# Kernel tuning notes

Hardware: AMD Instinct MI355X
Metric: run time of the kernel (lower is better)

The kernel has to match this reference:

```python
import jax, jax.numpy as jnp
import numpy as np
import math

B, S, E, H = 2, 2048, 1024, 16
D = E // H
EPS = 1e-5


def setup_inputs() -> dict:
    key = jax.random.key(0)
    ks = jax.random.split(key, 6)
    s = 1.0 / math.sqrt(E)
    return {
        "query": jax.random.normal(ks[0], (B, S, E), jnp.float32),
        "Wq": jax.random.normal(ks[1], (E, E), jnp.float32) * s,
        "bq": jnp.zeros((E,), jnp.float32),
        "Wk": jax.random.normal(ks[2], (E, E), jnp.float32) * s,
        "bk": jnp.zeros((E,), jnp.float32),
        "Wv": jax.random.normal(ks[3], (E, E), jnp.float32) * s,
        "bv": jnp.zeros((E,), jnp.float32),
        "Wo": jax.random.normal(ks[4], (E, E), jnp.float32) * s,
        "bo": jnp.zeros((E,), jnp.float32),
        "alpha": jnp.ones((1,), jnp.float32),
    }


def reference(query, Wq, bq, Wk, bk, Wv, bv, Wo, bo, alpha):
    # Q/K/V projections (nn.Linear: x @ W.T + b)
    q = (query @ Wq.T + bq).reshape(B, S, H, D)
    k = (query @ Wk.T + bk).reshape(B, S, H, D)
    v = (query @ Wv.T + bv).reshape(B, S, H, D)

    # YAT scores: (q.k)^2 / (||q-k||^2 + eps)
    qk = jnp.einsum('bqhd,bkhd->bhqk', q, k)          # [B,H,S,S]
    sq = jnp.einsum('bqhd,bqhd->bhq', q, q)           # ||q||^2
    sk = jnp.einsum('bkhd,bkhd->bhk', k, k)           # ||k||^2
    dist_sq = sq[..., :, None] + sk[..., None, :] - 2.0 * qk
    scores = (qk * qk) / (dist_sq + EPS)

    # learnable alpha scaling: scores * (sqrt(d)/log(1+d))^alpha
    scale = (jnp.sqrt(jnp.float32(D)) / jnp.log1p(jnp.float32(D))) ** alpha[0]
    scores = scores * scale

    attn = jax.nn.softmax(scores, axis=-1)
    out = jnp.einsum('bhqk,bkhd->bqhd', attn, v).reshape(B, S, E)
    return out @ Wo.T + bo
```

## Files before the change

kernel.cpp:

```cpp
#include <hip/hip_runtime.h>
#include <hip/hip_fp16.h>
#include <math.h>

#define BB 2
#define SS 2048
#define EE 1024
#define HH 16
#define DD 64
#define YAT_EPS 1e-5f
#define RR (BB * HH * SS)

typedef __attribute__((ext_vector_type(8))) short bf16x8;
typedef __attribute__((ext_vector_type(4))) short short4v;
typedef __attribute__((ext_vector_type(4))) float f32x4;
#define MFMA16(a, b, c) __builtin_amdgcn_mfma_f32_16x16x32_bf16((a), (b), (c), 0, 0, 0)

#if __has_builtin(__builtin_amdgcn_exp2f)
#define EXP2(x) __builtin_amdgcn_exp2f(x)
#else
#define EXP2(x) exp2f(x)
#endif
#if __has_builtin(__builtin_amdgcn_rcpf)
#define RCPF(x) __builtin_amdgcn_rcpf(x)
#else
#define RCPF(x) (1.0f / (x))
#endif

__device__ __forceinline__ unsigned short f2bf(float x) {
    unsigned int u = __float_as_uint(x);
    u += 0x7FFFu + ((u >> 16) & 1u);
    return (unsigned short)(u >> 16);
}
__device__ __forceinline__ float bf2f(unsigned short h) {
    return __uint_as_float(((unsigned int)h) << 16);
}
__device__ __forceinline__ short f2bf_t(float x) {
    return (short)(__float_as_uint(x) >> 16);
}

__device__ __forceinline__ void async_ld16(void* lds, const void* g) {
    __builtin_amdgcn_global_load_lds(
        (const __attribute__((address_space(1))) unsigned int*)g,
        (__attribute__((address_space(3))) unsigned int*)lds, 16, 0, 0);
}

__global__ __launch_bounds__(256) void split_f32(const float* __restrict__ in,
                                                 unsigned short* __restrict__ hi,
                                                 unsigned short* __restrict__ lo,
                                                 int n4) {
    int i = blockIdx.x * 256 + threadIdx.x;
    if (i >= n4) return;
    float4 v = ((const float4*)in)[i];
    ushort4 h, l;
    h.x = f2bf(v.x); l.x = f2bf(v.x - bf2f(h.x));
    h.y = f2bf(v.y); l.y = f2bf(v.y - bf2f(h.y));
    h.z = f2bf(v.z); l.z = f2bf(v.z - bf2f(h.z));
    h.w = f2bf(v.w); l.w = f2bf(v.w - bf2f(h.w));
    ((ushort4*)hi)[i] = h;
    ((ushort4*)lo)[i] = l;
}

__global__ __launch_bounds__(256) void split_w4(
        const float* __restrict__ Wq, const float* __restrict__ Wk,
        const float* __restrict__ Wv, const float* __restrict__ Wo,
        unsigned short* __restrict__ Whi, unsigned short* __restrict__ Wlo,
        unsigned short* __restrict__ Wohi) {
    int i = blockIdx.x * 256 + threadIdx.x;
    int y = blockIdx.y;
    const float* src = y == 0 ? Wq : y == 1 ? Wk : y == 2 ? Wv : Wo;
    unsigned short* hi = y < 3 ? Whi + (size_t)y * EE * EE : Wohi;
    float4 v = ((const float4*)src)[i];
    ushort4 h;
    h.x = f2bf(v.x); h.y = f2bf(v.y); h.z = f2bf(v.z); h.w = f2bf(v.w);
    ((ushort4*)hi)[i] = h;
    if (y < 2) {
        unsigned short* lo = Wlo + (size_t)y * EE * EE;
        ushort4 l;
        l.x = f2bf(v.x - bf2f(h.x));
        l.y = f2bf(v.y - bf2f(h.y));
        l.z = f2bf(v.z - bf2f(h.z));
        l.w = f2bf(v.w - bf2f(h.w));
        ((ushort4*)lo)[i] = l;
    }
}

__global__ __launch_bounds__(256, 2) void proj_qkv(
        const unsigned short* __restrict__ Ahi, const unsigned short* __restrict__ Alo,
        const unsigned short* __restrict__ Whi, const unsigned short* __restrict__ Wlo,
        const float* __restrict__ bq, const float* __restrict__ bk,
        const float* __restrict__ bv,
        unsigned short* __restrict__ qhi, unsigned short* __restrict__ qlo,
        unsigned short* __restrict__ khi, unsigned short* __restrict__ vt,
        float* __restrict__ sqn, float* __restrict__ skn) {
    __shared__ __align__(16) unsigned short SH[128 * 136];
    unsigned short* LA_hi = SH;
    unsigned short* LA_lo = SH + 4096;
    unsigned short* LB_hi = SH + 8192;
    unsigned short* LB_lo = SH + 12288;

    const int K = EE;
    const int t = threadIdx.x;
    const int w = t >> 6, lane = t & 63;
    const int quad = lane >> 4, lr = lane & 15;
    const int wy = w & 1, wx = w >> 1;
    const bool p3 = blockIdx.x < 16;
    const int m0 = blockIdx.y * 128;
    const int n0 = p3 ? blockIdx.x * 128 : 0;
    const int c0 = p3 ? 0 : (blockIdx.x - 16) * 128;

    const unsigned short* gsrc = nullptr;
    unsigned short* ldst = nullptr;
    if (w == 0)      { gsrc = Ahi + (size_t)m0 * K; ldst = LA_hi; }
    else if (w == 2) {
        gsrc = p3 ? Whi + (size_t)n0 * K
                  : Whi + (size_t)(2 * EE + c0) * K;
        ldst = LB_hi;
    } else if (p3 && w == 1) { gsrc = Alo + (size_t)m0 * K; ldst = LA_lo; }
    else if (p3 && w == 3)   { gsrc = Wlo + (size_t)n0 * K; ldst = LB_lo; }
    const unsigned short* gl = gsrc ? gsrc + (size_t)(lane >> 2) * K + (lane & 3) * 8
                                    : nullptr;

    f32x4 acc[4][4];
    #pragma unroll
    for (int i = 0; i < 4; ++i)
        #pragma unroll
        for (int j = 0; j < 4; ++j)
            acc[i][j] = (f32x4){0.f, 0.f, 0.f, 0.f};

    for (int k0 = 0; k0 < K; k0 += 32) {
        __syncthreads();
        if (gl) {
            #pragma unroll
            for (int i = 0; i < 8; ++i)
                async_ld16(ldst + i * 512, gl + (size_t)i * 16 * K + k0);
        }
        __syncthreads();
        bf16x8 ah[4], al[4], bh_[4], bl_[4];
        #pragma unroll
        for (int i = 0; i < 4; ++i) {
            ah[i]  = *(const bf16x8*)&LA_hi[(wy * 64 + i * 16 + lr) * 32 + quad * 8];
            bh_[i] = *(const bf16x8*)&LB_hi[(wx * 64 + i * 16 + lr) * 32 + quad * 8];
            if (p3) {
                al[i]  = *(const bf16x8*)&LA_lo[(wy * 64 + i * 16 + lr) * 32 + quad * 8];
                bl_[i] = *(const bf16x8*)&LB_lo[(wx * 64 + i * 16 + lr) * 32 + quad * 8];
            }
        }
        #pragma unroll
        for (int mg = 0; mg < 4; ++mg)
            #pragma unroll
            for (int ns = 0; ns < 4; ++ns) {
                f32x4 a = acc[mg][ns];
                a = MFMA16(ah[mg], bh_[ns], a);
                if (p3) {
                    a = MFMA16(ah[mg], bl_[ns], a);
                    a = MFMA16(al[mg], bh_[ns], a);
                }
                acc[mg][ns] = a;
            }
    }

    if (p3) {
        const int ng = n0 + wx * 64;
        const int path = ng >> 10;
        const int c = ng & 1023;
        const int h = c >> 6;
        const float* bias = path == 0 ? bq : bk;
        unsigned short* hi_p = path == 0 ? qhi : khi;
        float* nrm = path == 0 ? sqn : skn;
        float bias_v[4];
        #pragma unroll
        for (int ns = 0; ns < 4; ++ns) bias_v[ns] = bias[c + ns * 16 + lr];
        #pragma unroll
        for (int mg = 0; mg < 4; ++mg)
            #pragma unroll
            for (int r = 0; r < 4; ++r) {
                int m = m0 + wy * 64 + mg * 16 + quad * 4 + r;
                int b = m >> 11, s = m & (SS - 1);
                size_t base = ((size_t)(b * HH + h) * SS + s) * DD;
                float v4[4];
                #pragma unroll
                for (int ns = 0; ns < 4; ++ns) v4[ns] = acc[mg][ns][r] + bias_v[ns];
                float pn = v4[0] * v4[0] + v4[1] * v4[1] + v4[2] * v4[2] + v4[3] * v4[3];
                #pragma unroll
                for (int off = 1; off < 16; off <<= 1) pn += __shfl_xor(pn, off);
                if (lr == 0) nrm[(size_t)(b * HH + h) * SS + s] = pn;
                #pragma unroll
                for (int ns = 0; ns < 4; ++ns) {
                    unsigned short hv = f2bf(v4[ns]);
                    hi_p[base + ns * 16 + lr] = hv;
                    if (path == 0)
                        qlo[base + ns * 16 + lr] = f2bf(v4[ns] - bf2f(hv));
                }
            }
    } else {
        __syncthreads();
        float bias_v[4];
        #pragma unroll
        for (int ns = 0; ns < 4; ++ns) bias_v[ns] = bv[c0 + wx * 64 + ns * 16 + lr];
        #pragma unroll
        for (int mg = 0; mg < 4; ++mg)
            #pragma unroll
            for (int r = 0; r < 4; ++r) {
                int mloc = wy * 64 + mg * 16 + quad * 4 + r;
                #pragma unroll
                for (int ns = 0; ns < 4; ++ns) {
                    int cloc = wx * 64 + ns * 16 + lr;
                    SH[cloc * 136 + mloc] = f2bf(acc[mg][ns][r] + bias_v[ns]);
                }
            }
        __syncthreads();
        const int b = m0 >> 11, s0 = m0 & (SS - 1);
        #pragma unroll
        for (int jc = 0; jc < 8; ++jc) {
            int cl = (t >> 4) + jc * 16;
            int sl = (t & 15) * 8;
            bf16x8 vv = *(const bf16x8*)&SH[cl * 136 + sl];
            int c = c0 + cl, h = c >> 6, d = c & 63;
            *(bf16x8*)&vt[((size_t)(b * HH + h) * DD + d) * SS + s0 + sl] = vv;
        }
    }
}

template <int MODE, int PASSES>
__global__ __launch_bounds__(256, 2) void gemm3p(
        const unsigned short* __restrict__ Ahi, const unsigned short* __restrict__ Alo,
        const unsigned short* __restrict__ Bhi, const unsigned short* __restrict__ Blo,
        const float* __restrict__ bq,
        float* __restrict__ Cf,
        int M, int N, int K) {
    __shared__ __align__(16) unsigned short LA_hi[128 * 32];
    __shared__ __align__(16) unsigned short LB_hi[128 * 32];

    const int t = threadIdx.x;
    const int w = t >> 6, lane = t & 63;
    const int quad = lane >> 4, lr = lane & 15;
    const int wy = w & 1, wx = w >> 1;
    const int m0 = blockIdx.y * 128, n0 = blockIdx.x * 128;

    const unsigned short* gsrc = nullptr;
    unsigned short* ldst = nullptr;
    if (w == 0)      { gsrc = Ahi + (size_t)m0 * K; ldst = LA_hi; }
    else if (w == 2) { gsrc = Bhi + (size_t)n0 * K; ldst = LB_hi; }
    const unsigned short* gl = gsrc ? gsrc + (size_t)(lane >> 2) * K + (lane & 3) * 8
                                    : nullptr;

    f32x4 acc[4][4];
    #pragma unroll
    for (int i = 0; i < 4; ++i)
        #pragma unroll
        for (int j = 0; j < 4; ++j)
            acc[i][j] = (f32x4){0.f, 0.f, 0.f, 0.f};

    for (int k0 = 0; k0 < K; k0 += 32) {
        __syncthreads();
        if (gl) {
            #pragma unroll
            for (int i = 0; i < 8; ++i)
                async_ld16(ldst + i * 512, gl + (size_t)i * 16 * K + k0);
        }
        __syncthreads();
        bf16x8 ah[4], bh_[4];
        #pragma unroll
        for (int i = 0; i < 4; ++i) {
            ah[i]  = *(const bf16x8*)&LA_hi[(wy * 64 + i * 16 + lr) * 32 + quad * 8];
            bh_[i] = *(const bf16x8*)&LB_hi[(wx * 64 + i * 16 + lr) * 32 + quad * 8];
        }
        #pragma unroll
        for (int mg = 0; mg < 4; ++mg)
            #pragma unroll
            for (int ns = 0; ns < 4; ++ns)
                acc[mg][ns] = MFMA16(ah[mg], bh_[ns], acc[mg][ns]);
    }

    const int ng = n0 + wx * 64;
    float bias_v[4];
    #pragma unroll
    for (int ns = 0; ns < 4; ++ns) bias_v[ns] = bq[ng + ns * 16 + lr];
    #pragma unroll
    for (int mg = 0; mg < 4; ++mg)
        #pragma unroll
        for (int r = 0; r < 4; ++r) {
            int m = m0 + wy * 64 + mg * 16 + quad * 4 + r;
            #pragma unroll
            for (int ns = 0; ns < 4; ++ns)
                Cf[(size_t)m * N + ng + ns * 16 + lr] = acc[mg][ns][r] + bias_v[ns];
        }
}

__global__ __launch_bounds__(256, 4) void yat_attn_mfma(
        const unsigned short* __restrict__ qhi, const unsigned short* __restrict__ qlo,
        const unsigned short* __restrict__ khi,
        const unsigned short* __restrict__ vt,
        const float* __restrict__ sqn, const float* __restrict__ skn,
        const float* __restrict__ alphap,
        __half* __restrict__ Opart, float2* __restrict__ mlpart) {
    __shared__ __align__(16) unsigned short Ks[2][4096];
    __shared__ __align__(16) unsigned short Ps[4][16 * 68];

    const int t = threadIdx.x;
    const int w = t >> 6, lane = t & 63;
    const int quad = lane >> 4, lr = lane & 15;
    const int qt = blockIdx.x, bh = blockIdx.y, z = blockIdx.z;
    const int row0 = qt * 64 + w * 16;
    const float cscale = powf(sqrtf((float)DD) / log1pf((float)DD), alphap[0])
                         * 1.4426950408889634f;

    bf16x8 qh[2], ql[2];
    #pragma unroll
    for (int kd = 0; kd < 2; ++kd) {
        size_t o = ((size_t)bh * SS + row0 + lr) * DD + kd * 32 + quad * 8;
        qh[kd] = *(const bf16x8*)&qhi[o];
        ql[kd] = *(const bf16x8*)&qlo[o];
    }
    const float sqe = sqn[(size_t)bh * SS + row0 + lr] + YAT_EPS;

    const int lrow = lane >> 3;
    const int lofs = lrow * 64 + (((lane & 7) ^ (lrow & 7)) << 3);
    const int sw = lr & 7;

    float m_r = -INFINITY, l_r = 0.f;
    f32x4 O[4];
    #pragma unroll
    for (int nd = 0; nd < 4; ++nd) O[nd] = (f32x4){0.f, 0.f, 0.f, 0.f};

    const int t0 = z * 16;
    const size_t khi_base = (size_t)bh * SS * 64 + (size_t)w * 16 * 64 + lofs;
    const size_t skn_base = (size_t)bh * SS + quad * 4;
    unsigned short* myP = Ps[w];

    #pragma unroll
    for (int i2 = 0; i2 < 2; ++i2)
        async_ld16(&Ks[0][w * 1024 + i2 * 512],
                   khi + khi_base + (size_t)t0 * 4096 + i2 * 512);

    for (int it = 0; it < 16; ++it) {
        const int p = it & 1;
        __syncthreads();
        if (it + 1 < 16) {
            #pragma unroll
            for (int i2 = 0; i2 < 2; ++i2)
                async_ld16(&Ks[p ^ 1][w * 1024 + i2 * 512],
                           khi + khi_base + (size_t)(t0 + it + 1) * 4096 + i2 * 512);
        }
        const int kbase = (t0 + it) * 64;
        const unsigned short* kb = Ks[p];
        f32x4 acc[4];
        f32x4 sk4[4];
        #pragma unroll
        for (int st = 0; st < 4; ++st) {
            const int rbase = (st * 16 + lr) * 64;
            bf16x8 kh0 = *(const bf16x8*)&kb[rbase + ((quad    ) ^ sw) * 8];
            bf16x8 kh1 = *(const bf16x8*)&kb[rbase + ((quad + 4) ^ sw) * 8];
            sk4[st] = *(const f32x4*)&skn[skn_base + kbase + st * 16];
            f32x4 a = (f32x4){0.f, 0.f, 0.f, 0.f};
            a = MFMA16(kh0, qh[0], a);
            a = MFMA16(kh1, qh[1], a);
            a = MFMA16(kh0, ql[0], a);
            a = MFMA16(kh1, ql[1], a);
            acc[st] = a;
        }
        bf16x8 vf[4][2];
        #pragma unroll
        for (int nd = 0; nd < 4; ++nd)
            #pragma unroll
            for (int kk = 0; kk < 2; ++kk)
                vf[nd][kk] = *(const bf16x8*)&vt[((size_t)bh * DD + nd * 16 + lr) * SS
                                                 + kbase + kk * 32 + quad * 8];
        float mx = -INFINITY;
        #pragma unroll
        for (int st = 0; st < 4; ++st)
            #pragma unroll
            for (int r = 0; r < 4; ++r) {
                float qk = acc[st][r];
                float d = sqe + sk4[st][r] - 2.f * qk;
                float u = qk * qk * RCPF(d);
                acc[st][r] = u;
                mx = fmaxf(mx, u);
            }
        mx = fmaxf(mx, __shfl_xor(mx, 16));
        mx = fmaxf(mx, __shfl_xor(mx, 32));
        float mnew = fmaxf(m_r, mx);
        bool resc = !__all(cscale * (mnew - m_r) <= 8.f);
        float aa = 1.f;
        if (resc) {
            aa = EXP2(__builtin_fmaf(cscale, m_r, -cscale * mnew));
            m_r = mnew;
        }
        const float cm = cscale * m_r;
        float rs = 0.f;
        #pragma unroll
        for (int st = 0; st < 4; ++st) {
            float e0 = EXP2(__builtin_fmaf(cscale, acc[st][0], -cm));
            float e1 = EXP2(__builtin_fmaf(cscale, acc[st][1], -cm));
            float e2 = EXP2(__builtin_fmaf(cscale, acc[st][2], -cm));
            float e3 = EXP2(__builtin_fmaf(cscale, acc[st][3], -cm));
            rs += (e0 + e1) + (e2 + e3);
            short4v pv;
            pv[0] = f2bf_t(e0); pv[1] = f2bf_t(e1);
            pv[2] = f2bf_t(e2); pv[3] = f2bf_t(e3);
            *(short4v*)&myP[lr * 68 + st * 16 + quad * 4] = pv;
        }
        rs += __shfl_xor(rs, 16);
        rs += __shfl_xor(rs, 32);
        l_r = l_r * aa + rs;
        if (resc) {
            float al_[4];
            #pragma unroll
            for (int r = 0; r < 4; ++r) al_[r] = __shfl(aa, quad * 4 + r);
            #pragma unroll
            for (int nd = 0; nd < 4; ++nd)
                #pragma unroll
                for (int r = 0; r < 4; ++r)
                    O[nd][r] *= al_[r];
        }
        bf16x8 pf[2];
        #pragma unroll
        for (int kk = 0; kk < 2; ++kk)
            pf[kk] = *(const bf16x8*)&myP[lr * 68 + kk * 32 + quad * 8];
        #pragma unroll
        for (int nd = 0; nd < 4; ++nd)
            #pragma unroll
            for (int kk = 0; kk < 2; ++kk)
                O[nd] = MFMA16(pf[kk], vf[nd][kk], O[nd]);
    }
    if (quad == 0)
        mlpart[(size_t)z * RR + (size_t)bh * SS + row0 + lr] =
            make_float2(cscale * m_r, l_r);
    #pragma unroll
    for (int r = 0; r < 4; ++r) {
        size_t rowg = (size_t)bh * SS + row0 + quad * 4 + r;
        #pragma unroll
        for (int nd = 0; nd < 4; ++nd)
            Opart[((size_t)z * RR + rowg) * DD + nd * 16 + lr] =
                __float2half(O[nd][r]);
    }
}

__global__ __launch_bounds__(256) void combine_attn(
        const __half* __restrict__ Opart, const float2* __restrict__ mlpart,
        unsigned short* __restrict__ ctxhi) {
    int tid = blockIdx.x * 256 + threadIdx.x;
    int row = tid >> 4, c4 = (tid & 15) * 4;
    float2 ml0 = mlpart[row];
    float2 ml1 = mlpart[RR + row];
    float ms = fmaxf(ml0.x, ml1.x);
    float a0 = EXP2(ml0.x - ms), a1 = EXP2(ml1.x - ms);
    float inv = RCPF(ml0.y * a0 + ml1.y * a1);
    a0 *= inv; a1 *= inv;
    const __half* p0 = Opart + (size_t)row * DD + c4;
    const __half* p1 = p0 + (size_t)RR * DD;
    int bh = row >> 11, s = row & (SS - 1);
    int b = bh >> 4, h = bh & 15;
    size_t idx = ((size_t)b * SS + s) * EE + h * DD + c4;
    ushort4 hv;
    unsigned short* hp = (unsigned short*)&hv;
    #pragma unroll
    for (int j = 0; j < 4; ++j) {
        float o = __half2float(p0[j]) * a0 + __half2float(p1[j]) * a1;
        hp[j] = f2bf(o);
    }
    *(ushort4*)&ctxhi[idx] = hv;
}

extern "C" void kernel_launch(void* const* d_in, const int* in_sizes, int n_in,
                              void* d_out, int out_size, void* d_ws, size_t ws_size,
                              hipStream_t stream) {
    const float* x     = (const float*)d_in[0];
    const float* Wq    = (const float*)d_in[1];
    const float* bq    = (const float*)d_in[2];
    const float* Wk    = (const float*)d_in[3];
    const float* bk    = (const float*)d_in[4];
    const float* Wv    = (const float*)d_in[5];
    const float* bv    = (const float*)d_in[6];
    const float* Wo    = (const float*)d_in[7];
    const float* bo    = (const float*)d_in[8];
    const float* alpha = (const float*)d_in[9];
    float* out = (float*)d_out;
    char* ws = (char*)d_ws;

    const int M = BB * SS;
    const size_t MB = 1u << 20;
    unsigned short* xhi  = (unsigned short*)(ws + 0 * MB);
    unsigned short* xlo  = (unsigned short*)(ws + 8 * MB);
    unsigned short* Whi  = (unsigned short*)(ws + 16 * MB);
    unsigned short* Wlo  = (unsigned short*)(ws + 22 * MB);
    float2* mlpart       = (float2*)(ws + 24 * MB);
    unsigned short* Wohi = (unsigned short*)(ws + 28 * MB);
    unsigned short* qhi  = (unsigned short*)(ws + 32 * MB);
    unsigned short* qlo  = (unsigned short*)(ws + 40 * MB);
    unsigned short* khi  = (unsigned short*)(ws + 48 * MB);
    unsigned short* vt   = (unsigned short*)(ws + 56 * MB);
    __half* Opart        = (__half*)(ws + 64 * MB);
    float* sqn = (float*)(ws + 80 * MB);
    float* skn = (float*)(ws + 80 * MB + 256 * 1024);
    unsigned short* ctxhi = xhi;

    const int nX = M * EE / 4, nW = EE * EE / 4;
    split_f32<<<nX / 256, 256, 0, stream>>>(x, xhi, xlo, nX);
    split_w4<<<dim3(nW / 256, 4), 256, 0, stream>>>(Wq, Wk, Wv, Wo, Whi, Wlo, Wohi);

    proj_qkv<<<dim3(24, M / 128), 256, 0, stream>>>(
        xhi, xlo, Whi, Wlo, bq, bk, bv,
        qhi, qlo, khi, vt, sqn, skn);

    yat_attn_mfma<<<dim3(SS / 64, BB * HH, 2), 256, 0, stream>>>(
        qhi, qlo, khi, vt, sqn, skn, alpha, Opart, mlpart);

    combine_attn<<<RR * 16 / 256, 256, 0, stream>>>(Opart, mlpart, ctxhi);

    gemm3p<0, 1><<<dim3(EE / 128, M / 128), 256, 0, stream>>>(
        ctxhi, nullptr, Wohi, nullptr, bo, out, M, EE, EE);
}
```

Baseline: 329.3 us.

## Drop split-K attention and combine kernel; merge input split kernels

The attention kernel no longer splits the key range in two. Each block now walks all 32 key tiles and writes the normalized bf16 context directly, which removes the fp16 partial-output buffer, the max/sum buffer and the separate combine kernel. The two fp32-to-bf16 split kernels are also merged into one launch. In exchange the attention grid has half as many blocks (1024 instead of 2048) with twice the work each, which can reduce parallelism and latency hiding.

Measured after the change: 320.7 us, median of 4. -2.6%, faster.

```diff
diff --git a/kernel.cpp b/kernel.cpp
--- a/kernel.cpp
+++ b/kernel.cpp
@@ -44,43 +44,43 @@
         (__attribute__((address_space(3))) unsigned int*)lds, 16, 0, 0);
 }
 
-__global__ __launch_bounds__(256) void split_f32(const float* __restrict__ in,
-                                                 unsigned short* __restrict__ hi,
-                                                 unsigned short* __restrict__ lo,
-                                                 int n4) {
-    int i = blockIdx.x * 256 + threadIdx.x;
-    if (i >= n4) return;
-    float4 v = ((const float4*)in)[i];
-    ushort4 h, l;
-    h.x = f2bf(v.x); l.x = f2bf(v.x - bf2f(h.x));
-    h.y = f2bf(v.y); l.y = f2bf(v.y - bf2f(h.y));
-    h.z = f2bf(v.z); l.z = f2bf(v.z - bf2f(h.z));
-    h.w = f2bf(v.w); l.w = f2bf(v.w - bf2f(h.w));
-    ((ushort4*)hi)[i] = h;
-    ((ushort4*)lo)[i] = l;
-}
-
-__global__ __launch_bounds__(256) void split_w4(
+__global__ __launch_bounds__(256) void split_all(
+        const float* __restrict__ x,
         const float* __restrict__ Wq, const float* __restrict__ Wk,
         const float* __restrict__ Wv, const float* __restrict__ Wo,
+        unsigned short* __restrict__ xhi, unsigned short* __restrict__ xlo,
         unsigned short* __restrict__ Whi, unsigned short* __restrict__ Wlo,
         unsigned short* __restrict__ Wohi) {
-    int i = blockIdx.x * 256 + threadIdx.x;
-    int y = blockIdx.y;
-    const float* src = y == 0 ? Wq : y == 1 ? Wk : y == 2 ? Wv : Wo;
-    unsigned short* hi = y < 3 ? Whi + (size_t)y * EE * EE : Wohi;
-    float4 v = ((const float4*)src)[i];
-    ushort4 h;
-    h.x = f2bf(v.x); h.y = f2bf(v.y); h.z = f2bf(v.z); h.w = f2bf(v.w);
-    ((ushort4*)hi)[i] = h;
-    if (y < 2) {
-        unsigned short* lo = Wlo + (size_t)y * EE * EE;
-        ushort4 l;
-        l.x = f2bf(v.x - bf2f(h.x));
-        l.y = f2bf(v.y - bf2f(h.y));
-        l.z = f2bf(v.z - bf2f(h.z));
-        l.w = f2bf(v.w - bf2f(h.w));
-        ((ushort4*)lo)[i] = l;
+    const int bid = blockIdx.x;
+    if (bid < 4096) {
+        int i = bid * 256 + threadIdx.x;
+        float4 v = ((const float4*)x)[i];
+        ushort4 h, l;
+        h.x = f2bf(v.x); l.x = f2bf(v.x - bf2f(h.x));
+        h.y = f2bf(v.y); l.y = f2bf(v.y - bf2f(h.y));
+        h.z = f2bf(v.z); l.z = f2bf(v.z - bf2f(h.z));
+        h.w = f2bf(v.w); l.w = f2bf(v.w - bf2f(h.w));
+        ((ushort4*)xhi)[i] = h;
+        ((ushort4*)xlo)[i] = l;
+    } else {
+        int idx = bid - 4096;
+        int y = idx >> 10;
+        int i = (idx & 1023) * 256 + threadIdx.x;
+        const float* src = y == 0 ? Wq : y == 1 ? Wk : y == 2 ? Wv : Wo;
+        unsigned short* hi = y < 3 ? Whi + (size_t)y * EE * EE : Wohi;
+        float4 v = ((const float4*)src)[i];
+        ushort4 h;
+        h.x = f2bf(v.x); h.y = f2bf(v.y); h.z = f2bf(v.z); h.w = f2bf(v.w);
+        ((ushort4*)hi)[i] = h;
+        if (y < 2) {
+            unsigned short* lo = Wlo + (size_t)y * EE * EE;
+            ushort4 l;
+            l.x = f2bf(v.x - bf2f(h.x));
+            l.y = f2bf(v.y - bf2f(h.y));
+            l.z = f2bf(v.z - bf2f(h.z));
+            l.w = f2bf(v.w - bf2f(h.w));
+            ((ushort4*)lo)[i] = l;
+        }
     }
 }
 
@@ -221,10 +221,9 @@
     }
 }
 
-template <int MODE, int PASSES>
-__global__ __launch_bounds__(256, 2) void gemm3p(
-        const unsigned short* __restrict__ Ahi, const unsigned short* __restrict__ Alo,
-        const unsigned short* __restrict__ Bhi, const unsigned short* __restrict__ Blo,
+__global__ __launch_bounds__(256, 2) void gemm_o(
+        const unsigned short* __restrict__ Ahi,
+        const unsigned short* __restrict__ Bhi,
         const float* __restrict__ bq,
         float* __restrict__ Cf,
         int M, int N, int K) {
@@ -293,14 +292,14 @@
         const unsigned short* __restrict__ vt,
         const float* __restrict__ sqn, const float* __restrict__ skn,
         const float* __restrict__ alphap,
-        __half* __restrict__ Opart, float2* __restrict__ mlpart) {
+        unsigned short* __restrict__ ctxhi) {
     __shared__ __align__(16) unsigned short Ks[2][4096];
     __shared__ __align__(16) unsigned short Ps[4][16 * 68];
 
     const int t = threadIdx.x;
     const int w = t >> 6, lane = t & 63;
     const int quad = lane >> 4, lr = lane & 15;
-    const int qt = blockIdx.x, bh = blockIdx.y, z = blockIdx.z;
+    const int qt = blockIdx.x, bh = blockIdx.y;
     const int row0 = qt * 64 + w * 16;
     const float cscale = powf(sqrtf((float)DD) / log1pf((float)DD), alphap[0])
                          * 1.4426950408889634f;
@@ -323,26 +322,24 @@
     #pragma unroll
     for (int nd = 0; nd < 4; ++nd) O[nd] = (f32x4){0.f, 0.f, 0.f, 0.f};
 
-    const int t0 = z * 16;
     const size_t khi_base = (size_t)bh * SS * 64 + (size_t)w * 16 * 64 + lofs;
     const size_t skn_base = (size_t)bh * SS + quad * 4;
     unsigned short* myP = Ps[w];
 
     #pragma unroll
     for (int i2 = 0; i2 < 2; ++i2)
-        async_ld16(&Ks[0][w * 1024 + i2 * 512],
-                   khi + khi_base + (size_t)t0 * 4096 + i2 * 512);
-
-    for (int it = 0; it < 16; ++it) {
+        async_ld16(&Ks[0][w * 1024 + i2 * 512], khi + khi_base + i2 * 512);
+
+    for (int it = 0; it < 32; ++it) {
         const int p = it & 1;
         __syncthreads();
-        if (it + 1 < 16) {
+        if (it + 1 < 32) {
             #pragma unroll
             for (int i2 = 0; i2 < 2; ++i2)
                 async_ld16(&Ks[p ^ 1][w * 1024 + i2 * 512],
-                           khi + khi_base + (size_t)(t0 + it + 1) * 4096 + i2 * 512);
-        }
-        const int kbase = (t0 + it) * 64;
+                           khi + khi_base + (size_t)(it + 1) * 4096 + i2 * 512);
+        }
+        const int kbase = it * 64;
         const unsigned short* kb = Ks[p];
         f32x4 acc[4];
         f32x4 sk4[4];
@@ -423,43 +420,17 @@
             for (int kk = 0; kk < 2; ++kk)
                 O[nd] = MFMA16(pf[kk], vf[nd][kk], O[nd]);
     }
-    if (quad == 0)
-        mlpart[(size_t)z * RR + (size_t)bh * SS + row0 + lr] =
-            make_float2(cscale * m_r, l_r);
+    const int b = bh >> 4, h = bh & 15;
     #pragma unroll
     for (int r = 0; r < 4; ++r) {
-        size_t rowg = (size_t)bh * SS + row0 + quad * 4 + r;
+        float li = __shfl(l_r, quad * 4 + r);
+        float inv = RCPF(li);
+        int s = row0 + quad * 4 + r;
+        size_t base = ((size_t)b * SS + s) * EE + h * DD;
         #pragma unroll
         for (int nd = 0; nd < 4; ++nd)
-            Opart[((size_t)z * RR + rowg) * DD + nd * 16 + lr] =
-                __float2half(O[nd][r]);
-    }
-}
-
-__global__ __launch_bounds__(256) void combine_attn(
-        const __half* __restrict__ Opart, const float2* __restrict__ mlpart,
-        unsigned short* __restrict__ ctxhi) {
-    int tid = blockIdx.x * 256 + threadIdx.x;
-    int row = tid >> 4, c4 = (tid & 15) * 4;
-    float2 ml0 = mlpart[row];
-    float2 ml1 = mlpart[RR + row];
-    float ms = fmaxf(ml0.x, ml1.x);
-    float a0 = EXP2(ml0.x - ms), a1 = EXP2(ml1.x - ms);
-    float inv = RCPF(ml0.y * a0 + ml1.y * a1);
-    a0 *= inv; a1 *= inv;
-    const __half* p0 = Opart + (size_t)row * DD + c4;
-    const __half* p1 = p0 + (size_t)RR * DD;
-    int bh = row >> 11, s = row & (SS - 1);
-    int b = bh >> 4, h = bh & 15;
-    size_t idx = ((size_t)b * SS + s) * EE + h * DD + c4;
-    ushort4 hv;
-    unsigned short* hp = (unsigned short*)&hv;
-    #pragma unroll
-    for (int j = 0; j < 4; ++j) {
-        float o = __half2float(p0[j]) * a0 + __half2float(p1[j]) * a1;
-        hp[j] = f2bf(o);
-    }
-    *(ushort4*)&ctxhi[idx] = hv;
+            ctxhi[base + nd * 16 + lr] = f2bf(O[nd][r] * inv);
+    }
 }
 
 extern "C" void kernel_launch(void* const* d_in, const int* in_sizes, int n_in,
@@ -484,30 +455,25 @@
     unsigned short* xlo  = (unsigned short*)(ws + 8 * MB);
     unsigned short* Whi  = (unsigned short*)(ws + 16 * MB);
     unsigned short* Wlo  = (unsigned short*)(ws + 22 * MB);
-    float2* mlpart       = (float2*)(ws + 24 * MB);
     unsigned short* Wohi = (unsigned short*)(ws + 28 * MB);
     unsigned short* qhi  = (unsigned short*)(ws + 32 * MB);
     unsigned short* qlo  = (unsigned short*)(ws + 40 * MB);
     unsigned short* khi  = (unsigned short*)(ws + 48 * MB);
     unsigned short* vt   = (unsigned short*)(ws + 56 * MB);
-    __half* Opart        = (__half*)(ws + 64 * MB);
     float* sqn = (float*)(ws + 80 * MB);
     float* skn = (float*)(ws + 80 * MB + 256 * 1024);
     unsigned short* ctxhi = xhi;
 
-    const int nX = M * EE / 4, nW = EE * EE / 4;
-    split_f32<<<nX / 256, 256, 0, stream>>>(x, xhi, xlo, nX);
-    split_w4<<<dim3(nW / 256, 4), 256, 0, stream>>>(Wq, Wk, Wv, Wo, Whi, Wlo, Wohi);
+    split_all<<<8192, 256, 0, stream>>>(x, Wq, Wk, Wv, Wo,
+                                        xhi, xlo, Whi, Wlo, Wohi);
 
     proj_qkv<<<dim3(24, M / 128), 256, 0, stream>>>(
         xhi, xlo, Whi, Wlo, bq, bk, bv,
         qhi, qlo, khi, vt, sqn, skn);
 
-    yat_attn_mfma<<<dim3(SS / 64, BB * HH, 2), 256, 0, stream>>>(
-        qhi, qlo, khi, vt, sqn, skn, alpha, Opart, mlpart);
-
-    combine_attn<<<RR * 16 / 256, 256, 0, stream>>>(Opart, mlpart, ctxhi);
-
-    gemm3p<0, 1><<<dim3(EE / 128, M / 128), 256, 0, stream>>>(
-        ctxhi, nullptr, Wohi, nullptr, bo, out, M, EE, EE);
-}
+    yat_attn_mfma<<<dim3(SS / 64, BB * HH), 256, 0, stream>>>(
+        qhi, qlo, khi, vt, sqn, skn, alpha, ctxhi);
+
+    gemm_o<<<dim3(EE / 128, M / 128), 256, 0, stream>>>(
+        ctxhi, Wohi, bo, out, M, EE, EE);
+}
```
